# Optimization experiments

Measured on AMD Instinct MI355X. Metric: run time of the kernel, lower is better.

The kernel has to match this reference:

```python
import jax, jax.numpy as jnp
import numpy as np

B = 128
IN = 256
NLVL = 6
KLVL = 3
CH = 4
C = 4 * CH * CH          # 64 channels per node
OU = 8                   # out_filter_siz_u
OV = 8                   # out_filter_siz_v
NK = 2 ** KLVL           # 8 leaf nodes per axis
W_SCALE = 1.0 / 16.0     # ~1/sqrt(2*2*C) so 7 stacked relu-convs stay numerically sane


def setup_inputs() -> dict:
    key = jax.random.key(0)
    ks = jax.random.split(key, 2 * NLVL + 4)
    fx = IN // 2 ** NLVL  # 4: input patch filter size
    inp = {}
    inp["in_data"] = jax.random.normal(ks[0], (B, IN, IN, 1), jnp.float32)
    inp["in_filter"] = jax.random.normal(ks[1], (fx, fx, 1, C), jnp.float32) * W_SCALE
    inp["in_bias"] = jnp.zeros((C,), jnp.float32)
    i = 2
    for lvl in range(1, NLVL + 1):
        n = 2 ** min(lvl, KLVL)  # node grid: grows to 2^klvl then stays
        inp[f"f{lvl}"] = jax.random.normal(ks[i], (n, n, 2, 2, C, C), jnp.float32) * W_SCALE
        inp[f"b{lvl}"] = jnp.zeros((n, n, C), jnp.float32)
        i += 1
    inp["Wd"] = jax.random.normal(ks[i], (NK, NK, 2, C, OU * OV), jnp.float32) * W_SCALE
    return inp


def _node_conv(x, w, b):
    # x: [Nu,Nv,B,H,W,C]; w: [Nu,Nv,2,2,C,C]; 2x2 stride-2 VALID conv per node
    Nu, Nv, Bn, H, W, Cc = x.shape
    xr = x.reshape(Nu, Nv, Bn, H // 2, 2, W // 2, 2, Cc)
    y = jnp.einsum('uvbhxwyc,uvxyco->uvbhwo', xr, w)
    return jax.nn.relu(y + b[:, :, None, None, None, :])


def _forward(in_data, in_filter, in_bias, fs, bs, Wd):
    Bn = in_data.shape[0]
    fx, fy = in_filter.shape[0], in_filter.shape[1]
    # input interp conv: stride == kernel -> non-overlapping patch GEMM
    xr = in_data[..., 0].reshape(Bn, in_data.shape[1] // fx, fx, in_data.shape[2] // fy, fy)
    x = jax.nn.relu(jnp.einsum('bxpyq,pqc->bxyc', xr, in_filter[:, :, 0, :]) + in_bias)
    x = x[None, None]  # [1,1,B,2^nlvl,2^nlvl,C] node grid
    for lvl in range(1, NLVL + 1):
        if lvl <= KLVL:
            # children (itu,itv) read parent (itu//2, itv//2)
            x = jnp.repeat(jnp.repeat(x, 2, axis=0), 2, axis=1)
        x = _node_conv(x, fs[lvl - 1], bs[lvl - 1])
    feats = x[:, :, :, 0, 0, :]  # [NK,NK,B,C]; spatial is 1x1 at level nlvl
    out = jnp.einsum('uvbc,uvrck->uvbrk', feats, Wd)  # r in {real, imag}
    out = out.reshape(NK, NK, Bn, 2, OU, OV)
    out = jnp.transpose(out, (2, 0, 4, 1, 5, 3))  # [B,itu,ou,itv,ov,2]
    return out.reshape(Bn, NK * OU, NK * OV, 2)


def reference(in_data, in_filter, in_bias, f1, b1, f2, b2, f3, b3, f4, b4, f5, b5, f6, b6, Wd):
    fs = (f1, f2, f3, f4, f5, f6)
    bs = (b1, b2, b3, b4, b5, b6)
    return _forward(in_data, in_filter, in_bias, fs, bs, Wd)
```

## Files before the change

### kernel.cpp

```cpp
#include <hip/hip_runtime.h>
#include <hip/hip_bf16.h>
#include <cstdint>
#include <cstddef>


typedef __attribute__((ext_vector_type(8))) short short8;
typedef __attribute__((ext_vector_type(4))) float f32x4;
typedef unsigned short ushort_t;

static __device__ __forceinline__ float b2f(const __hip_bfloat16 x) {
    return __bfloat162float(x);
}
static __device__ __forceinline__ ushort_t f2bf(float x) {
    __hip_bfloat16 h = __float2bfloat16(x);
    ushort_t u;
    __builtin_memcpy(&u, &h, 2);
    return u;
}
static __device__ __forceinline__ void gl_lds16(const void* g, void* l) {
    __builtin_amdgcn_global_load_lds(
        (const __attribute__((address_space(1))) void*)g,
        (__attribute__((address_space(3))) void*)l, 16, 0, 0);
}
#define WAIT_LGKM0() __builtin_amdgcn_s_waitcnt(0xC07F)
#define WAIT_VM0()   __builtin_amdgcn_s_waitcnt(0x0F70)

__global__ __launch_bounds__(256) void k_prep(
    const uint32_t* __restrict__ in_words,
    const void* f1, const void* f2, const void* f3,
    const void* f4, const void* f5, const void* f6, const void* wdsrc,
    const void* b1, const void* b2, const void* b3,
    const void* b4, const void* b5, const void* b6,
    ushort_t* __restrict__ wbuf, ushort_t* __restrict__ wdbuf,
    float* __restrict__ bbuf, int* __restrict__ flag)
{
    __shared__ int sflag;
    const int t = threadIdx.x;
    if (t < 64) {
        const float v = __uint_as_float(in_words[t]);
        const bool plaus = (v == 0.0f) || (fabsf(v) > 1e-8f && fabsf(v) < 1e4f);
        const unsigned long long m = __ballot(plaus);
        if (t == 0) sflag = (__popcll(m) >= 48) ? 0 : 1;
    }
    __syncthreads();
    const int isbf = sflag;
    const int gid = blockIdx.x * 256 + t;
    if (blockIdx.x == 0 && t == 0) *flag = isbf;

    if (gid >= 648448) return;
    if (gid >= 630784) {
        const int bg = gid - 630784;
        const void* src; int base;
        if      (bg <   256) { src = b1; base = 0;     }
        else if (bg <  1280) { src = b2; base = 256;   }
        else if (bg <  5376) { src = b3; base = 1280;  }
        else if (bg <  9472) { src = b4; base = 5376;  }
        else if (bg < 13568) { src = b5; base = 9472;  }
        else                 { src = b6; base = 13568; }
        const int local = bg - base;
        bbuf[bg] = isbf ? b2f(((const __hip_bfloat16*)src)[local])
                        : ((const float*)src)[local];
        return;
    }
    if (gid >= 565248) {
        const int local = gid - 565248;
        const int lane = local & 63;
        const int slot = (local >> 6) & 15;
        const int site = local >> 10;
        const int ks2 = slot >> 3, nh = slot & 7, q = lane >> 4;
        const int n = nh * 16 + (lane & 15);
        const int r = n >> 6, kk = n & 63;
        const int cbase = ks2 * 32 + q * 8;
        ushort_t pk[8];
        if (isbf) {
            const ushort_t* s = (const ushort_t*)wdsrc;
            #pragma unroll
            for (int j = 0; j < 8; j++)
                pk[j] = s[(((size_t)(site * 2 + r) * 64 + cbase + j) * 64) + kk];
        } else {
            const float* s = (const float*)wdsrc;
            #pragma unroll
            for (int j = 0; j < 8; j++)
                pk[j] = f2bf(s[(((size_t)(site * 2 + r) * 64 + cbase + j) * 64) + kk]);
        }
        *(uint4*)&wdbuf[(size_t)local * 8] = *(uint4*)pk;
        return;
    }
    const void* fsrc; int base;
    if      (gid <   8192) { fsrc = f1; base = 0;      }
    else if (gid <  40960) { fsrc = f2; base = 8192;   }
    else if (gid < 172032) { fsrc = f3; base = 40960;  }
    else if (gid < 303104) { fsrc = f4; base = 172032; }
    else if (gid < 434176) { fsrc = f5; base = 303104; }
    else                   { fsrc = f6; base = 434176; }
    const int local = gid - base;
    const int lane = local & 63;
    const int slot = (local >> 6) & 7;
    const int sitetap = local >> 9;
    const int ks = slot >> 2, nh = slot & 3, q = lane >> 4;
    const int n = (lane & 15) + nh * 16;
    const int kbase = ks * 32 + q * 8;
    ushort_t pk[8];
    if (isbf) {
        const ushort_t* s = (const ushort_t*)fsrc + (size_t)sitetap * 4096;
        #pragma unroll
        for (int j = 0; j < 8; j++) pk[j] = s[(kbase + j) * 64 + n];
    } else {
        const float* s = (const float*)fsrc + (size_t)sitetap * 4096;
        #pragma unroll
        for (int j = 0; j < 8; j++) pk[j] = f2bf(s[(kbase + j) * 64 + n]);
    }
    *(uint4*)&wbuf[(size_t)gid * 8] = *(uint4*)pk;
}

__global__ __launch_bounds__(256) void k_stage0(
    const void* __restrict__ in_data, const void* __restrict__ filt,
    const void* __restrict__ bias, __hip_bfloat16* __restrict__ x0,
    const int* __restrict__ flag, int b_off)
{
    const int isbf = *flag;
    const int blk = blockIdx.x;
    const int X  = blk & 63;
    const int bl = blk >> 6;
    const int bg = bl + b_off;

    __shared__ float sIn[4][256];
    __shared__ float sF[16][64];
    __shared__ float sB[64];

    const int t = threadIdx.x;
    const size_t srow = ((size_t)bg * 256 + (size_t)X * 4) * 256;

    if (isbf) {
        const __hip_bfloat16* src = (const __hip_bfloat16*)in_data + srow;
        #pragma unroll
        for (int i = 0; i < 4; i++) {
            int flat = i * 256 + t;
            int p = flat >> 8, col = flat & 255;
            sIn[p][col] = b2f(src[(size_t)p * 256 + col]);
        }
        const __hip_bfloat16* fsrc = (const __hip_bfloat16*)filt;
        #pragma unroll
        for (int i = 0; i < 4; i++) {
            int flat = i * 256 + t;
            sF[flat >> 6][flat & 63] = b2f(fsrc[flat]);
        }
        if (t < 64) sB[t] = b2f(((const __hip_bfloat16*)bias)[t]);
    } else {
        const float* src = (const float*)in_data + srow;
        const int p = t >> 6, c4 = (t & 63) * 4;
        *(float4*)&sIn[p][c4] = *(const float4*)(src + (size_t)p * 256 + c4);
        const float* fsrc = (const float*)filt;
        #pragma unroll
        for (int i = 0; i < 4; i++) {
            int flat = i * 256 + t;
            sF[flat >> 6][flat & 63] = fsrc[flat];
        }
        if (t < 64) sB[t] = ((const float*)bias)[t];
    }
    __syncthreads();

    const int ty = t >> 4;
    const int tc = t & 15;

    float acc[4][4];
    {
        const float4 bv = *(const float4*)&sB[tc * 4];
        #pragma unroll
        for (int yi = 0; yi < 4; yi++) {
            acc[yi][0] = bv.x; acc[yi][1] = bv.y;
            acc[yi][2] = bv.z; acc[yi][3] = bv.w;
        }
    }

    #pragma unroll
    for (int p = 0; p < 4; p++) {
        float4 rin[4], rf[4];
        #pragma unroll
        for (int yi = 0; yi < 4; yi++)
            rin[yi] = *(const float4*)&sIn[p][ty * 16 + yi * 4];
        #pragma unroll
        for (int q = 0; q < 4; q++)
            rf[q] = *(const float4*)&sF[p * 4 + q][tc * 4];
        #pragma unroll
        for (int yi = 0; yi < 4; yi++) {
            #pragma unroll
            for (int q = 0; q < 4; q++) {
                const float a = ((const float*)&rin[yi])[q];
                acc[yi][0] = fmaf(a, rf[q].x, acc[yi][0]);
                acc[yi][1] = fmaf(a, rf[q].y, acc[yi][1]);
                acc[yi][2] = fmaf(a, rf[q].z, acc[yi][2]);
                acc[yi][3] = fmaf(a, rf[q].w, acc[yi][3]);
            }
        }
    }

    ushort_t* dst = (ushort_t*)(x0 + ((size_t)bl * 64 + X) * 64 * 64);
    #pragma unroll
    for (int yi = 0; yi < 4; yi++) {
        uint2 pk;
        pk.x = (uint32_t)f2bf(fmaxf(acc[yi][0], 0.f))
             | ((uint32_t)f2bf(fmaxf(acc[yi][1], 0.f)) << 16);
        pk.y = (uint32_t)f2bf(fmaxf(acc[yi][2], 0.f))
             | ((uint32_t)f2bf(fmaxf(acc[yi][3], 0.f)) << 16);
        *(uint2*)(dst + (size_t)(ty * 4 + yi) * 64 + tc * 4) = pk;
    }
}

__global__ __launch_bounds__(256) void k_level4(
    const __hip_bfloat16* __restrict__ xin,
    const ushort_t* __restrict__ wbuf,
    const float* __restrict__ bbuf,
    __hip_bfloat16* __restrict__ xout,
    int Nv_out, int HW, int Bc, int mtiles)
{
    __shared__ ushort_t smem[20480];
    __shared__ float sBias[4][64];
    ushort_t* sA = smem;
    ushort_t* sB = smem + 4096;

    int idx = blockIdx.x;
    const int mt = idx % mtiles; idx /= mtiles;
    const int w  = idx % HW; idx /= HW;
    const int h  = idx % HW; idx /= HW;
    const int Nv_in = Nv_out >> 1;
    const int vp = idx % Nv_in;
    const int up = idx / Nv_in;

    const int t = threadIdx.x;
    const int wave = t >> 6, lane = t & 63;
    const int lm = lane & 15, lq = lane >> 4;

    {
        const int ct = t >> 6, o = t & 63;
        const int so_t = (2 * up + (ct >> 1)) * Nv_out + (2 * vp + (ct & 1));
        sBias[ct][o] = bbuf[so_t * 64 + o];
    }

    const int so = (2 * up + (wave >> 1)) * Nv_out + (2 * vp + (wave & 1));
    const int H_in = HW * 2;
    const size_t bstride = (size_t)H_in * H_in * 64;
    const size_t siteb = (size_t)(up * Nv_in + vp) * Bc * bstride;
    const ushort_t* wsite = wbuf + (size_t)so * 4 * 4096;

    const f32x4 zero = {0.f, 0.f, 0.f, 0.f};
    f32x4 acc[4][4];
    #pragma unroll
    for (int i = 0; i < 4; i++)
        #pragma unroll
        for (int j = 0; j < 4; j++) acc[i][j] = zero;

    for (int tap = 0; tap < 4; tap++) {
        const int hi = 2 * h + (tap >> 1), wi = 2 * w + (tap & 1);
        const size_t tapoff = siteb + ((size_t)hi * H_in + wi) * 64;
        #pragma unroll
        for (int s2 = 0; s2 < 2; s2++) {
            const int s = wave * 2 + s2;
            const int ks = s >> 2, mh = s & 3;
            int b = mt * 64 + lm + mh * 16;
            if (b >= Bc) b = Bc - 1;
            gl_lds16(xin + tapoff + (size_t)b * bstride + ks * 32 + lq * 8,
                     &sA[s * 512]);
        }
        const ushort_t* wt = wsite + (size_t)tap * 4096;
        #pragma unroll
        for (int s = 0; s < 8; s++) {
            gl_lds16(wt + s * 512 + lane * 8, &sB[wave * 4096 + s * 512]);
        }
        __syncthreads();

        #pragma unroll
        for (int ks = 0; ks < 2; ks++) {
            short8 bf0 = *(const short8*)&sB[wave * 4096 + (ks * 4 + 0) * 512 + lane * 8];
            short8 bf1 = *(const short8*)&sB[wave * 4096 + (ks * 4 + 1) * 512 + lane * 8];
            short8 bf2 = *(const short8*)&sB[wave * 4096 + (ks * 4 + 2) * 512 + lane * 8];
            short8 bf3 = *(const short8*)&sB[wave * 4096 + (ks * 4 + 3) * 512 + lane * 8];
            #pragma unroll
            for (int fm = 0; fm < 4; fm++) {
                short8 a = *(const short8*)&sA[(ks * 4 + fm) * 512 + lane * 8];
                acc[fm][0] = __builtin_amdgcn_mfma_f32_16x16x32_bf16(a, bf0, acc[fm][0], 0, 0, 0);
                acc[fm][1] = __builtin_amdgcn_mfma_f32_16x16x32_bf16(a, bf1, acc[fm][1], 0, 0, 0);
                acc[fm][2] = __builtin_amdgcn_mfma_f32_16x16x32_bf16(a, bf2, acc[fm][2], 0, 0, 0);
                acc[fm][3] = __builtin_amdgcn_mfma_f32_16x16x32_bf16(a, bf3, acc[fm][3], 0, 0, 0);
            }
        }
        __syncthreads();
    }

    float bv[4];
    #pragma unroll
    for (int fn = 0; fn < 4; fn++) bv[fn] = sBias[wave][fn * 16 + lm];
    ushort_t* so_buf = smem + wave * 4352;
    #pragma unroll
    for (int fm = 0; fm < 4; fm++) {
        #pragma unroll
        for (int fn = 0; fn < 4; fn++) {
            #pragma unroll
            for (int r = 0; r < 4; r++) {
                const int row = fm * 16 + lq * 4 + r;
                so_buf[row * 68 + fn * 16 + lm] =
                    f2bf(fmaxf(acc[fm][fn][r] + bv[fn], 0.f));
            }
        }
    }
    __syncthreads();

    const size_t ostride = (size_t)HW * HW * 64;
    const size_t obase = (size_t)so * Bc * ostride + ((size_t)h * HW + w) * 64;
    #pragma unroll
    for (int i = 0; i < 8; i++) {
        const int task = i * 64 + lane;
        const int oct = task & 7, row = task >> 3;
        const int b = mt * 64 + row;
        if (b < Bc) {
            *(uint4*)(xout + obase + (size_t)b * ostride + oct * 8) =
                *(const uint4*)&so_buf[row * 68 + oct * 8];
        }
    }
}

__global__ __launch_bounds__(256, 1) void k_f456(
    const __hip_bfloat16* __restrict__ xin,
    const ushort_t* __restrict__ w4, const ushort_t* __restrict__ w5,
    const ushort_t* __restrict__ w6, const ushort_t* __restrict__ wd,
    const float* __restrict__ b4, const float* __restrict__ b5,
    const float* __restrict__ b6,
    void* __restrict__ out, const int* __restrict__ flag,
    int Bc, int b_off, int mtiles)
{
    const int isbf = *flag;
    const int bx = blockIdx.x;
    const int mt = bx % mtiles;
    const int site = bx / mtiles;
    const int u = site >> 3, v = site & 7;

    __shared__ ushort_t smem[74752];
    __shared__ float sBias[192];

    const int t = threadIdx.x;
    const int wv = t >> 6, lane = t & 63;
    const int lm = lane & 15, lq = lane >> 4;

    if (t < 64) {
        sBias[t]       = b4[site * 64 + t];
        sBias[64 + t]  = b5[site * 64 + t];
        sBias[128 + t] = b6[site * 64 + t];
    }

    {
        const ushort_t* w4s = w4 + (size_t)site * 16384;
        const ushort_t* w5s = w5 + (size_t)site * 16384;
        #pragma unroll
        for (int s2 = 0; s2 < 8; s2++) {
            const int s = wv * 8 + s2;
            gl_lds16(w4s + s * 512 + lane * 8, &smem[s * 512]);
            gl_lds16(w5s + s * 512 + lane * 8, &smem[16384 + s * 512]);
        }
    }
    __syncthreads();

    const f32x4 zero = {0.f, 0.f, 0.f, 0.f};
    const int h5 = wv >> 1, w5p = wv & 1;
    ushort_t* mid1w = smem + 32768 + wv * 8448;
    ushort_t* Aw = smem + 66560 + wv * 2048;
    const size_t sb = (size_t)site * Bc;

    for (int i = 0; i < 4; i++) {
        const int h4 = 2 * h5 + (i >> 1), w4p = 2 * w5p + (i & 1);
        f32x4 acc[2][4];
        #pragma unroll
        for (int a_ = 0; a_ < 2; a_++)
            #pragma unroll
            for (int b_ = 0; b_ < 4; b_++) acc[a_][b_] = zero;

        for (int tap = 0; tap < 4; tap++) {
            const int h3 = 2 * h4 + (tap >> 1), w3 = 2 * w4p + (tap & 1);
            WAIT_LGKM0();
            #pragma unroll
            for (int sl = 0; sl < 4; sl++) {
                const int ks = sl >> 1, mh = sl & 1;
                int b = mt * 32 + mh * 16 + lm;
                if (b >= Bc) b = Bc - 1;
                gl_lds16(xin + (sb + b) * 4096 + (h3 * 8 + w3) * 64 + ks * 32 + lq * 8,
                         &Aw[sl * 512]);
            }
            WAIT_VM0();
            #pragma unroll
            for (int ks = 0; ks < 2; ks++) {
                #pragma unroll
                for (int fm = 0; fm < 2; fm++) {
                    short8 a = *(const short8*)&Aw[(ks * 2 + fm) * 512 + lane * 8];
                    #pragma unroll
                    for (int fn = 0; fn < 4; fn++) {
                        short8 bfr = *(const short8*)&smem[(tap * 8 + ks * 4 + fn) * 512 + lane * 8];
                        acc[fm][fn] = __builtin_amdgcn_mfma_f32_16x16x32_bf16(a, bfr, acc[fm][fn], 0, 0, 0);
                    }
                }
            }
        }
        #pragma unroll
        for (int fm = 0; fm < 2; fm++) {
            #pragma unroll
            for (int fn = 0; fn < 4; fn++) {
                #pragma unroll
                for (int r = 0; r < 4; r++) {
                    const int m = fm * 16 + lq * 4 + r;
                    const int ch = fn * 16 + lm;
                    mid1w[m * 264 + i * 64 + ch] =
                        f2bf(fmaxf(acc[fm][fn][r] + sBias[ch], 0.f));
                }
            }
        }
    }

    {
        f32x4 acc2[2][4];
        #pragma unroll
        for (int a_ = 0; a_ < 2; a_++)
            #pragma unroll
            for (int b_ = 0; b_ < 4; b_++) acc2[a_][b_] = zero;

        #pragma unroll
        for (int i = 0; i < 4; i++) {
            #pragma unroll
            for (int ks = 0; ks < 2; ks++) {
                short8 a0 = *(const short8*)&mid1w[lm * 264 + i * 64 + ks * 32 + lq * 8];
                short8 a1 = *(const short8*)&mid1w[(16 + lm) * 264 + i * 64 + ks * 32 + lq * 8];
                #pragma unroll
                for (int fn = 0; fn < 4; fn++) {
                    short8 bfr = *(const short8*)&smem[16384 + (i * 8 + ks * 4 + fn) * 512 + lane * 8];
                    acc2[0][fn] = __builtin_amdgcn_mfma_f32_16x16x32_bf16(a0, bfr, acc2[0][fn], 0, 0, 0);
                    acc2[1][fn] = __builtin_amdgcn_mfma_f32_16x16x32_bf16(a1, bfr, acc2[1][fn], 0, 0, 0);
                }
            }
        }
        #pragma unroll
        for (int fm = 0; fm < 2; fm++) {
            #pragma unroll
            for (int fn = 0; fn < 4; fn++) {
                #pragma unroll
                for (int r = 0; r < 4; r++) {
                    const int m = fm * 16 + lq * 4 + r;
                    const int ch = fn * 16 + lm;
                    mid1w[m * 72 + ch] =
                        f2bf(fmaxf(acc2[fm][fn][r] + sBias[64 + ch], 0.f));
                }
            }
        }
    }
    __syncthreads();

    {
        const ushort_t* w6s = w6 + (size_t)site * 16384;
        const ushort_t* wds = wd + (size_t)site * 8192;
        #pragma unroll
        for (int s2 = 0; s2 < 8; s2++) {
            const int s = wv * 8 + s2;
            gl_lds16(w6s + s * 512 + lane * 8, &smem[s * 512]);
        }
        #pragma unroll
        for (int s2 = 0; s2 < 4; s2++) {
            const int s = wv * 4 + s2;
            gl_lds16(wds + s * 512 + lane * 8, &smem[16384 + s * 512]);
        }
    }
    __syncthreads();

    {
        f32x4 acc3[2];
        acc3[0] = zero; acc3[1] = zero;
        #pragma unroll
        for (int tap = 0; tap < 4; tap++) {
            const ushort_t* sl = smem + 32768 + tap * 8448;
            #pragma unroll
            for (int ks = 0; ks < 2; ks++) {
                short8 a0 = *(const short8*)&sl[lm * 72 + ks * 32 + lq * 8];
                short8 a1 = *(const short8*)&sl[(16 + lm) * 72 + ks * 32 + lq * 8];
                short8 bfr = *(const short8*)&smem[(tap * 8 + ks * 4 + wv) * 512 + lane * 8];
                acc3[0] = __builtin_amdgcn_mfma_f32_16x16x32_bf16(a0, bfr, acc3[0], 0, 0, 0);
                acc3[1] = __builtin_amdgcn_mfma_f32_16x16x32_bf16(a1, bfr, acc3[1], 0, 0, 0);
            }
        }
        ushort_t* mid3 = smem + 66560;
        #pragma unroll
        for (int fm = 0; fm < 2; fm++) {
            #pragma unroll
            for (int r = 0; r < 4; r++) {
                const int m = fm * 16 + lq * 4 + r;
                const int ch = wv * 16 + lm;
                mid3[m * 72 + ch] =
                    f2bf(fmaxf(acc3[fm][r] + sBias[128 + ch], 0.f));
            }
        }
    }
    __syncthreads();

    {
        const ushort_t* mid3 = smem + 66560;
        f32x4 acc4[2][2];
        acc4[0][0] = zero; acc4[0][1] = zero; acc4[1][0] = zero; acc4[1][1] = zero;
        #pragma unroll
        for (int ks = 0; ks < 2; ks++) {
            short8 a0 = *(const short8*)&mid3[lm * 72 + ks * 32 + lq * 8];
            short8 a1 = *(const short8*)&mid3[(16 + lm) * 72 + ks * 32 + lq * 8];
            #pragma unroll
            for (int n2 = 0; n2 < 2; n2++) {
                const int nh = 2 * wv + n2;
                short8 bfr = *(const short8*)&smem[16384 + (ks * 8 + nh) * 512 + lane * 8];
                acc4[0][n2] = __builtin_amdgcn_mfma_f32_16x16x32_bf16(a0, bfr, acc4[0][n2], 0, 0, 0);
                acc4[1][n2] = __builtin_amdgcn_mfma_f32_16x16x32_bf16(a1, bfr, acc4[1][n2], 0, 0, 0);
            }
        }
        #pragma unroll
        for (int fm = 0; fm < 2; fm++) {
            #pragma unroll
            for (int n2 = 0; n2 < 2; n2++) {
                const int n = (2 * wv + n2) * 16 + lm;
                const int rr = n >> 6, ou = (n >> 3) & 7, ov = n & 7;
                const size_t obase =
                    (((size_t)(u * 8 + ou)) * 64 + (v * 8 + ov)) * 2 + rr;
                #pragma unroll
                for (int reg = 0; reg < 4; reg++) {
                    const int brow = mt * 32 + fm * 16 + lq * 4 + reg;
                    if (brow < Bc) {
                        const size_t oidx = obase + (size_t)(b_off + brow) * 8192;
                        if (isbf) ((__hip_bfloat16*)out)[oidx] =
                            __float2bfloat16(acc4[fm][n2][reg]);
                        else ((float*)out)[oidx] = acc4[fm][n2][reg];
                    }
                }
            }
        }
    }
}

extern "C" void kernel_launch(void* const* d_in, const int* in_sizes, int n_in,
                              void* d_out, int out_size, void* d_ws, size_t ws_size,
                              hipStream_t stream)
{
    (void)in_sizes; (void)n_in; (void)out_size;

    const void* in_data = d_in[0];
    const void* filt    = d_in[1];
    const void* bias0   = d_in[2];
    const void* fl[7];
    const void* bl[7];
    for (int l = 1; l <= 6; l++) {
        fl[l] = d_in[1 + 2 * l];
        bl[l] = d_in[2 + 2 * l];
    }
    const void* Wd = d_in[15];

    const int Bfull = 128;
    const size_t perB = (size_t)64 * 64 * 64;

    const size_t wbufBytes  = 565248ull * 16;
    const size_t wdbufBytes = 65536ull * 16;
    const size_t bbufBytes  = 17664ull * 4;
    const size_t headBytes  = 256 + wbufBytes + wdbufBytes + bbufBytes;

    const size_t avail = ws_size > headBytes ? ws_size - headBytes : 0;
    int Bc = 0;
    for (int c = 128; c >= 1; c >>= 1) {
        if ((size_t)2 * c * perB * sizeof(__hip_bfloat16) <= avail) { Bc = c; break; }
    }
    if (Bc == 0) return;

    int* flag = (int*)d_ws;
    ushort_t* wbuf  = (ushort_t*)((char*)d_ws + 256);
    ushort_t* wdbuf = (ushort_t*)((char*)d_ws + 256 + wbufBytes);
    float* bbuf = (float*)((char*)d_ws + 256 + wbufBytes + wdbufBytes);
    __hip_bfloat16* bufA = (__hip_bfloat16*)((char*)d_ws + headBytes);
    __hip_bfloat16* bufB = bufA + (size_t)Bc * perB;

    static const size_t w_off[7] = {0, 0, 65536, 327680, 1376256, 2424832, 3473408};
    static const int    b_off_tab[7] = {0, 0, 256, 1280, 5376, 9472, 13568};

    k_prep<<<dim3(2533), 256, 0, stream>>>(
        (const uint32_t*)in_data,
        fl[1], fl[2], fl[3], fl[4], fl[5], fl[6], Wd,
        bl[1], bl[2], bl[3], bl[4], bl[5], bl[6],
        wbuf, wdbuf, bbuf, flag);

    const int mt4 = (Bc + 63) / 64;
    const int mt32 = (Bc + 31) / 32;

    for (int b_off = 0; b_off < Bfull; b_off += Bc) {
        k_stage0<<<dim3(Bc * 64), 256, 0, stream>>>(in_data, filt, bias0, bufA, flag, b_off);

        __hip_bfloat16* cur = bufA;
        __hip_bfloat16* nxt = bufB;
        for (int lvl = 1; lvl <= 3; lvl++) {
            const int Nu = 1 << lvl;
            const int H  = 64 >> lvl;
            const int Nv_in = Nu >> 1;
            dim3 grid(Nv_in * Nv_in * H * H * mt4);
            k_level4<<<grid, 256, 0, stream>>>(cur, wbuf + w_off[lvl],
                bbuf + b_off_tab[lvl], nxt, Nu, H, Bc, mt4);
            __hip_bfloat16* tmp = cur; cur = nxt; nxt = tmp;
        }

        k_f456<<<dim3(64 * mt32), 256, 0, stream>>>(cur,
            wbuf + w_off[4], wbuf + w_off[5], wbuf + w_off[6], wdbuf,
            bbuf + b_off_tab[4], bbuf + b_off_tab[5], bbuf + b_off_tab[6],
            d_out, flag, Bc, b_off, mt32);
    }
}
```

Baseline: 250.5 us.

## Fuse prep with stage0 and read weights directly into registers

```diff
diff --git a/kernel.cpp b/kernel.cpp
--- a/kernel.cpp
+++ b/kernel.cpp
@@ -22,31 +22,18 @@
         (const __attribute__((address_space(1))) void*)g,
         (__attribute__((address_space(3))) void*)l, 16, 0, 0);
 }
-#define WAIT_LGKM0() __builtin_amdgcn_s_waitcnt(0xC07F)
-#define WAIT_VM0()   __builtin_amdgcn_s_waitcnt(0x0F70)
-
-__global__ __launch_bounds__(256) void k_prep(
-    const uint32_t* __restrict__ in_words,
+
+#define PREP_BLOCKS 2533
+
+static __device__ __forceinline__ void prep_work(
+    int gid, int isbf,
     const void* f1, const void* f2, const void* f3,
     const void* f4, const void* f5, const void* f6, const void* wdsrc,
     const void* b1, const void* b2, const void* b3,
     const void* b4, const void* b5, const void* b6,
     ushort_t* __restrict__ wbuf, ushort_t* __restrict__ wdbuf,
-    float* __restrict__ bbuf, int* __restrict__ flag)
+    float* __restrict__ bbuf)
 {
-    __shared__ int sflag;
-    const int t = threadIdx.x;
-    if (t < 64) {
-        const float v = __uint_as_float(in_words[t]);
-        const bool plaus = (v == 0.0f) || (fabsf(v) > 1e-8f && fabsf(v) < 1e4f);
-        const unsigned long long m = __ballot(plaus);
-        if (t == 0) sflag = (__popcll(m) >= 48) ? 0 : 1;
-    }
-    __syncthreads();
-    const int isbf = sflag;
-    const int gid = blockIdx.x * 256 + t;
-    if (blockIdx.x == 0 && t == 0) *flag = isbf;
-
     if (gid >= 648448) return;
     if (gid >= 630784) {
         const int bg = gid - 630784;
@@ -113,13 +100,12 @@
     *(uint4*)&wbuf[(size_t)gid * 8] = *(uint4*)pk;
 }
 
-__global__ __launch_bounds__(256) void k_stage0(
+static __device__ __forceinline__ void stage0_body(
+    int blk, int isbf,
     const void* __restrict__ in_data, const void* __restrict__ filt,
     const void* __restrict__ bias, __hip_bfloat16* __restrict__ x0,
-    const int* __restrict__ flag, int b_off)
+    int b_off)
 {
-    const int isbf = *flag;
-    const int blk = blockIdx.x;
     const int X  = blk & 63;
     const int bl = blk >> 6;
     const int bg = bl + b_off;
@@ -207,17 +193,54 @@
     }
 }
 
-__global__ __launch_bounds__(256) void k_level4(
+__global__ __launch_bounds__(256) void k_prep0(
+    const void* __restrict__ in_data,
+    const void* f1, const void* f2, const void* f3,
+    const void* f4, const void* f5, const void* f6, const void* wdsrc,
+    const void* b1, const void* b2, const void* b3,
+    const void* b4, const void* b5, const void* b6,
+    ushort_t* __restrict__ wbuf, ushort_t* __restrict__ wdbuf,
+    float* __restrict__ bbuf, int* __restrict__ flag,
+    const void* __restrict__ filt, const void* __restrict__ bias0,
+    __hip_bfloat16* __restrict__ x0)
+{
+    __shared__ int sflag;
+    const int t = threadIdx.x;
+    if (t < 64) {
+        const float v = __uint_as_float(((const uint32_t*)in_data)[t]);
+        const bool plaus = (v == 0.0f) || (fabsf(v) > 1e-8f && fabsf(v) < 1e4f);
+        const unsigned long long m = __ballot(plaus);
+        if (t == 0) sflag = (__popcll(m) >= 48) ? 0 : 1;
+    }
+    __syncthreads();
+    const int isbf = sflag;
+
+    if (blockIdx.x < PREP_BLOCKS) {
+        if (blockIdx.x == 0 && t == 0) *flag = isbf;
+        prep_work(blockIdx.x * 256 + t, isbf,
+                  f1, f2, f3, f4, f5, f6, wdsrc,
+                  b1, b2, b3, b4, b5, b6, wbuf, wdbuf, bbuf);
+    } else {
+        stage0_body(blockIdx.x - PREP_BLOCKS, isbf, in_data, filt, bias0, x0, 0);
+    }
+}
+
+__global__ __launch_bounds__(256) void k_stage0(
+    const void* __restrict__ in_data, const void* __restrict__ filt,
+    const void* __restrict__ bias, __hip_bfloat16* __restrict__ x0,
+    const int* __restrict__ flag, int b_off)
+{
+    stage0_body(blockIdx.x, *flag, in_data, filt, bias, x0, b_off);
+}
+
+__global__ __launch_bounds__(256) void k_level_reg(
     const __hip_bfloat16* __restrict__ xin,
     const ushort_t* __restrict__ wbuf,
     const float* __restrict__ bbuf,
     __hip_bfloat16* __restrict__ xout,
     int Nv_out, int HW, int Bc, int mtiles)
 {
-    __shared__ ushort_t smem[20480];
-    __shared__ float sBias[4][64];
-    ushort_t* sA = smem;
-    ushort_t* sB = smem + 4096;
+    __shared__ ushort_t smem[17408];
 
     int idx = blockIdx.x;
     const int mt = idx % mtiles; idx /= mtiles;
@@ -231,17 +254,29 @@
     const int wave = t >> 6, lane = t & 63;
     const int lm = lane & 15, lq = lane >> 4;
 
-    {
-        const int ct = t >> 6, o = t & 63;
-        const int so_t = (2 * up + (ct >> 1)) * Nv_out + (2 * vp + (ct & 1));
-        sBias[ct][o] = bbuf[so_t * 64 + o];
-    }
-
     const int so = (2 * up + (wave >> 1)) * Nv_out + (2 * vp + (wave & 1));
     const int H_in = HW * 2;
     const size_t bstride = (size_t)H_in * H_in * 64;
     const size_t siteb = (size_t)(up * Nv_in + vp) * Bc * bstride;
-    const ushort_t* wsite = wbuf + (size_t)so * 4 * 4096;
+    const ushort_t* wsite = wbuf + (size_t)so * 4 * 4096 + lane * 8;
+
+    float bv[4];
+    #pragma unroll
+    for (int fn = 0; fn < 4; fn++) bv[fn] = bbuf[so * 64 + fn * 16 + lm];
+
+    {
+        const int hi = 2 * h + (wave >> 1), wi = 2 * w + (wave & 1);
+        const size_t tapoff = siteb + ((size_t)hi * H_in + wi) * 64;
+        #pragma unroll
+        for (int s2 = 0; s2 < 8; s2++) {
+            const int ks = s2 >> 2, mh = s2 & 3;
+            int b = mt * 64 + mh * 16 + lm;
+            if (b >= Bc) b = Bc - 1;
+            gl_lds16(xin + tapoff + (size_t)b * bstride + ks * 32 + lq * 8,
+                     &smem[(wave * 8 + s2) * 512]);
+        }
+    }
+    __syncthreads();
 
     const f32x4 zero = {0.f, 0.f, 0.f, 0.f};
     f32x4 acc[4][4];
@@ -250,46 +285,26 @@
         #pragma unroll
         for (int j = 0; j < 4; j++) acc[i][j] = zero;
 
+    #pragma unroll
     for (int tap = 0; tap < 4; tap++) {
-        const int hi = 2 * h + (tap >> 1), wi = 2 * w + (tap & 1);
-        const size_t tapoff = siteb + ((size_t)hi * H_in + wi) * 64;
-        #pragma unroll
-        for (int s2 = 0; s2 < 2; s2++) {
-            const int s = wave * 2 + s2;
-            const int ks = s >> 2, mh = s & 3;
-            int b = mt * 64 + lm + mh * 16;
-            if (b >= Bc) b = Bc - 1;
-            gl_lds16(xin + tapoff + (size_t)b * bstride + ks * 32 + lq * 8,
-                     &sA[s * 512]);
-        }
-        const ushort_t* wt = wsite + (size_t)tap * 4096;
-        #pragma unroll
-        for (int s = 0; s < 8; s++) {
-            gl_lds16(wt + s * 512 + lane * 8, &sB[wave * 4096 + s * 512]);
-        }
-        __syncthreads();
-
+        short8 B[8];
+        #pragma unroll
+        for (int s = 0; s < 8; s++)
+            B[s] = *(const short8*)(wsite + (tap * 8 + s) * 512);
         #pragma unroll
         for (int ks = 0; ks < 2; ks++) {
-            short8 bf0 = *(const short8*)&sB[wave * 4096 + (ks * 4 + 0) * 512 + lane * 8];
-            short8 bf1 = *(const short8*)&sB[wave * 4096 + (ks * 4 + 1) * 512 + lane * 8];
-            short8 bf2 = *(const short8*)&sB[wave * 4096 + (ks * 4 + 2) * 512 + lane * 8];
-            short8 bf3 = *(const short8*)&sB[wave * 4096 + (ks * 4 + 3) * 512 + lane * 8];
             #pragma unroll
             for (int fm = 0; fm < 4; fm++) {
-                short8 a = *(const short8*)&sA[(ks * 4 + fm) * 512 + lane * 8];
-                acc[fm][0] = __builtin_amdgcn_mfma_f32_16x16x32_bf16(a, bf0, acc[fm][0], 0, 0, 0);
-                acc[fm][1] = __builtin_amdgcn_mfma_f32_16x16x32_bf16(a, bf1, acc[fm][1], 0, 0, 0);
-                acc[fm][2] = __builtin_amdgcn_mfma_f32_16x16x32_bf16(a, bf2, acc[fm][2], 0, 0, 0);
-                acc[fm][3] = __builtin_amdgcn_mfma_f32_16x16x32_bf16(a, bf3, acc[fm][3], 0, 0, 0);
-            }
-        }
-        __syncthreads();
-    }
-
-    float bv[4];
-    #pragma unroll
-    for (int fn = 0; fn < 4; fn++) bv[fn] = sBias[wave][fn * 16 + lm];
+                short8 a = *(const short8*)&smem[(tap * 8 + ks * 4 + fm) * 512 + lane * 8];
+                #pragma unroll
+                for (int fn = 0; fn < 4; fn++)
+                    acc[fm][fn] = __builtin_amdgcn_mfma_f32_16x16x32_bf16(
+                        a, B[ks * 4 + fn], acc[fm][fn], 0, 0, 0);
+            }
+        }
+    }
+    __syncthreads();
+
     ushort_t* so_buf = smem + wave * 4352;
     #pragma unroll
     for (int fm = 0; fm < 4; fm++) {
@@ -334,36 +349,39 @@
     const int site = bx / mtiles;
     const int u = site >> 3, v = site & 7;
 
-    __shared__ ushort_t smem[74752];
-    __shared__ float sBias[192];
+    __shared__ ushort_t smem[36096];
 
     const int t = threadIdx.x;
     const int wv = t >> 6, lane = t & 63;
     const int lm = lane & 15, lq = lane >> 4;
 
-    if (t < 64) {
-        sBias[t]       = b4[site * 64 + t];
-        sBias[64 + t]  = b5[site * 64 + t];
-        sBias[128 + t] = b6[site * 64 + t];
-    }
-
-    {
-        const ushort_t* w4s = w4 + (size_t)site * 16384;
-        const ushort_t* w5s = w5 + (size_t)site * 16384;
-        #pragma unroll
-        for (int s2 = 0; s2 < 8; s2++) {
-            const int s = wv * 8 + s2;
-            gl_lds16(w4s + s * 512 + lane * 8, &smem[s * 512]);
-            gl_lds16(w5s + s * 512 + lane * 8, &smem[16384 + s * 512]);
-        }
-    }
-    __syncthreads();
+    const ushort_t* w4s = w4 + (size_t)site * 16384 + lane * 8;
+    const ushort_t* w5s = w5 + (size_t)site * 16384 + lane * 8;
+    const ushort_t* w6s = w6 + (size_t)site * 16384 + lane * 8;
+    const ushort_t* wds = wd + (size_t)site * 8192  + lane * 8;
+
+    float bv4[4], bv5[4];
+    #pragma unroll
+    for (int fn = 0; fn < 4; fn++) {
+        bv4[fn] = b4[site * 64 + fn * 16 + lm];
+        bv5[fn] = b5[site * 64 + fn * 16 + lm];
+    }
+    const float bv6 = b6[site * 64 + wv * 16 + lm];
 
     const f32x4 zero = {0.f, 0.f, 0.f, 0.f};
     const int h5 = wv >> 1, w5p = wv & 1;
-    ushort_t* mid1w = smem + 32768 + wv * 8448;
-    ushort_t* Aw = smem + 66560 + wv * 2048;
+    ushort_t* mid1w = smem + wv * 8448;
     const size_t sb = (size_t)site * Bc;
+
+    int brow[2];
+    #pragma unroll
+    for (int mh = 0; mh < 2; mh++) {
+        int b = mt * 32 + mh * 16 + lm;
+        if (b >= Bc) b = Bc - 1;
+        brow[mh] = b;
+    }
+    const __hip_bfloat16* xbase0 = xin + (sb + brow[0]) * 4096 + lq * 8;
+    const __hip_bfloat16* xbase1 = xin + (sb + brow[1]) * 4096 + lq * 8;
 
     for (int i = 0; i < 4; i++) {
         const int h4 = 2 * h5 + (i >> 1), w4p = 2 * w5p + (i & 1);
@@ -373,28 +391,19 @@
             #pragma unroll
             for (int b_ = 0; b_ < 4; b_++) acc[a_][b_] = zero;
 
+        #pragma unroll
         for (int tap = 0; tap < 4; tap++) {
             const int h3 = 2 * h4 + (tap >> 1), w3 = 2 * w4p + (tap & 1);
-            WAIT_LGKM0();
-            #pragma unroll
-            for (int sl = 0; sl < 4; sl++) {
-                const int ks = sl >> 1, mh = sl & 1;
-                int b = mt * 32 + mh * 16 + lm;
-                if (b >= Bc) b = Bc - 1;
-                gl_lds16(xin + (sb + b) * 4096 + (h3 * 8 + w3) * 64 + ks * 32 + lq * 8,
-                         &Aw[sl * 512]);
-            }
-            WAIT_VM0();
+            const int poff = (h3 * 8 + w3) * 64;
             #pragma unroll
             for (int ks = 0; ks < 2; ks++) {
+                short8 a0 = *(const short8*)(xbase0 + poff + ks * 32);
+                short8 a1 = *(const short8*)(xbase1 + poff + ks * 32);
                 #pragma unroll
-                for (int fm = 0; fm < 2; fm++) {
-                    short8 a = *(const short8*)&Aw[(ks * 2 + fm) * 512 + lane * 8];
-                    #pragma unroll
-                    for (int fn = 0; fn < 4; fn++) {
-                        short8 bfr = *(const short8*)&smem[(tap * 8 + ks * 4 + fn) * 512 + lane * 8];
-                        acc[fm][fn] = __builtin_amdgcn_mfma_f32_16x16x32_bf16(a, bfr, acc[fm][fn], 0, 0, 0);
-                    }
+                for (int fn = 0; fn < 4; fn++) {
+                    short8 bfr = *(const short8*)(w4s + (tap * 8 + ks * 4 + fn) * 512);
+                    acc[0][fn] = __builtin_amdgcn_mfma_f32_16x16x32_bf16(a0, bfr, acc[0][fn], 0, 0, 0);
+                    acc[1][fn] = __builtin_amdgcn_mfma_f32_16x16x32_bf16(a1, bfr, acc[1][fn], 0, 0, 0);
                 }
             }
         }
@@ -407,7 +416,7 @@
                     const int m = fm * 16 + lq * 4 + r;
                     const int ch = fn * 16 + lm;
                     mid1w[m * 264 + i * 64 + ch] =
-                        f2bf(fmaxf(acc[fm][fn][r] + sBias[ch], 0.f));
+                        f2bf(fmaxf(acc[fm][fn][r] + bv4[fn], 0.f));
                 }
             }
         }
@@ -428,7 +437,7 @@
                 short8 a1 = *(const short8*)&mid1w[(16 + lm) * 264 + i * 64 + ks * 32 + lq * 8];
                 #pragma unroll
                 for (int fn = 0; fn < 4; fn++) {
-                    short8 bfr = *(const short8*)&smem[16384 + (i * 8 + ks * 4 + fn) * 512 + lane * 8];
+                    short8 bfr = *(const short8*)(w5s + (i * 8 + ks * 4 + fn) * 512);
                     acc2[0][fn] = __builtin_amdgcn_mfma_f32_16x16x32_bf16(a0, bfr, acc2[0][fn], 0, 0, 0);
                     acc2[1][fn] = __builtin_amdgcn_mfma_f32_16x16x32_bf16(a1, bfr, acc2[1][fn], 0, 0, 0);
                 }
@@ -443,25 +452,9 @@
                     const int m = fm * 16 + lq * 4 + r;
                     const int ch = fn * 16 + lm;
                     mid1w[m * 72 + ch] =
-                        f2bf(fmaxf(acc2[fm][fn][r] + sBias[64 + ch], 0.f));
+                        f2bf(fmaxf(acc2[fm][fn][r] + bv5[fn], 0.f));
                 }
             }
-        }
-    }
-    __syncthreads();
-
-    {
-        const ushort_t* w6s = w6 + (size_t)site * 16384;
-        const ushort_t* wds = wd + (size_t)site * 8192;
-        #pragma unroll
-        for (int s2 = 0; s2 < 8; s2++) {
-            const int s = wv * 8 + s2;
-            gl_lds16(w6s + s * 512 + lane * 8, &smem[s * 512]);
-        }
-        #pragma unroll
-        for (int s2 = 0; s2 < 4; s2++) {
-            const int s = wv * 4 + s2;
-            gl_lds16(wds + s * 512 + lane * 8, &smem[16384 + s * 512]);
         }
     }
     __syncthreads();
@@ -471,17 +464,17 @@
         acc3[0] = zero; acc3[1] = zero;
         #pragma unroll
         for (int tap = 0; tap < 4; tap++) {
-            const ushort_t* sl = smem + 32768 + tap * 8448;
+            const ushort_t* sl = smem + tap * 8448;
             #pragma unroll
             for (int ks = 0; ks < 2; ks++) {
                 short8 a0 = *(const short8*)&sl[lm * 72 + ks * 32 + lq * 8];
                 short8 a1 = *(const short8*)&sl[(16 + lm) * 72 + ks * 32 + lq * 8];
-                short8 bfr = *(const short8*)&smem[(tap * 8 + ks * 4 + wv) * 512 + lane * 8];
+                short8 bfr = *(const short8*)(w6s + (tap * 8 + ks * 4 + wv) * 512);
                 acc3[0] = __builtin_amdgcn_mfma_f32_16x16x32_bf16(a0, bfr, acc3[0], 0, 0, 0);
                 acc3[1] = __builtin_amdgcn_mfma_f32_16x16x32_bf16(a1, bfr, acc3[1], 0, 0, 0);
             }
         }
-        ushort_t* mid3 = smem + 66560;
+        ushort_t* mid3 = smem + 33792;
         #pragma unroll
         for (int fm = 0; fm < 2; fm++) {
             #pragma unroll
@@ -489,14 +482,14 @@
                 const int m = fm * 16 + lq * 4 + r;
                 const int ch = wv * 16 + lm;
                 mid3[m * 72 + ch] =
-                    f2bf(fmaxf(acc3[fm][r] + sBias[128 + ch], 0.f));
+                    f2bf(fmaxf(acc3[fm][r] + bv6, 0.f));
             }
         }
     }
     __syncthreads();
 
     {
-        const ushort_t* mid3 = smem + 66560;
+        const ushort_t* mid3 = smem + 33792;
         f32x4 acc4[2][2];
         acc4[0][0] = zero; acc4[0][1] = zero; acc4[1][0] = zero; acc4[1][1] = zero;
         #pragma unroll
@@ -506,7 +499,7 @@
             #pragma unroll
             for (int n2 = 0; n2 < 2; n2++) {
                 const int nh = 2 * wv + n2;
-                short8 bfr = *(const short8*)&smem[16384 + (ks * 8 + nh) * 512 + lane * 8];
+                short8 bfr = *(const short8*)(wds + (ks * 8 + nh) * 512);
                 acc4[0][n2] = __builtin_amdgcn_mfma_f32_16x16x32_bf16(a0, bfr, acc4[0][n2], 0, 0, 0);
                 acc4[1][n2] = __builtin_amdgcn_mfma_f32_16x16x32_bf16(a1, bfr, acc4[1][n2], 0, 0, 0);
             }
@@ -521,9 +514,9 @@
                     (((size_t)(u * 8 + ou)) * 64 + (v * 8 + ov)) * 2 + rr;
                 #pragma unroll
                 for (int reg = 0; reg < 4; reg++) {
-                    const int brow = mt * 32 + fm * 16 + lq * 4 + reg;
-                    if (brow < Bc) {
-                        const size_t oidx = obase + (size_t)(b_off + brow) * 8192;
+                    const int brw = mt * 32 + fm * 16 + lq * 4 + reg;
+                    if (brw < Bc) {
+                        const size_t oidx = obase + (size_t)(b_off + brw) * 8192;
                         if (isbf) ((__hip_bfloat16*)out)[oidx] =
                             __float2bfloat16(acc4[fm][n2][reg]);
                         else ((float*)out)[oidx] = acc4[fm][n2][reg];
@@ -576,17 +569,20 @@
     static const size_t w_off[7] = {0, 0, 65536, 327680, 1376256, 2424832, 3473408};
     static const int    b_off_tab[7] = {0, 0, 256, 1280, 5376, 9472, 13568};
 
-    k_prep<<<dim3(2533), 256, 0, stream>>>(
-        (const uint32_t*)in_data,
-        fl[1], fl[2], fl[3], fl[4], fl[5], fl[6], Wd,
-        bl[1], bl[2], bl[3], bl[4], bl[5], bl[6],
-        wbuf, wdbuf, bbuf, flag);
-
     const int mt4 = (Bc + 63) / 64;
     const int mt32 = (Bc + 31) / 32;
 
     for (int b_off = 0; b_off < Bfull; b_off += Bc) {
-        k_stage0<<<dim3(Bc * 64), 256, 0, stream>>>(in_data, filt, bias0, bufA, flag, b_off);
+        if (b_off == 0) {
+            k_prep0<<<dim3(PREP_BLOCKS + Bc * 64), 256, 0, stream>>>(
+                in_data,
+                fl[1], fl[2], fl[3], fl[4], fl[5], fl[6], Wd,
+                bl[1], bl[2], bl[3], bl[4], bl[5], bl[6],
+                wbuf, wdbuf, bbuf, flag,
+                filt, bias0, bufA);
+        } else {
+            k_stage0<<<dim3(Bc * 64), 256, 0, stream>>>(in_data, filt, bias0, bufA, flag, b_off);
+        }
 
         __hip_bfloat16* cur = bufA;
         __hip_bfloat16* nxt = bufB;
@@ -595,7 +591,7 @@
             const int H  = 64 >> lvl;
             const int Nv_in = Nu >> 1;
             dim3 grid(Nv_in * Nv_in * H * H * mt4);
-            k_level4<<<grid, 256, 0, stream>>>(cur, wbuf + w_off[lvl],
+            k_level_reg<<<grid, 256, 0, stream>>>(cur, wbuf + w_off[lvl],
                 bbuf + b_off_tab[lvl], nxt, Nu, H, Bc, mt4);
             __hip_bfloat16* tmp = cur; cur = nxt; nxt = tmp;
         }
```

Measured after the change: 279.6 us. 1.12x slower.
